# Optimization experiments

Measured on AMD Instinct MI355X. Metric: run time of the kernel, lower is better.

Reference implementation:

```python
import math
import jax, jax.numpy as jnp
import numpy as np

NUM_HEADS = 16
HIDDEN = 1024
HEAD_SIZE = HIDDEN // NUM_HEADS
B, S = 4, 2048


def setup_inputs() -> dict:
    key = jax.random.key(0)
    k1, k2, k3 = jax.random.split(key, 3)
    scale = 1.0 / math.sqrt(HIDDEN)
    return {
        "hidden_states": jax.random.normal(k1, (B, S, HIDDEN), dtype=jnp.float32),
        "attention_mask": jnp.ones((B, S), dtype=jnp.float32),
        "Wq": jax.random.normal(k2, (HIDDEN, HIDDEN), dtype=jnp.float32) * scale,
        "bq": jnp.zeros((HIDDEN,), dtype=jnp.float32),
        "Wk": jax.random.normal(k3, (HIDDEN, HIDDEN), dtype=jnp.float32) * scale,
        "bk": jnp.zeros((HIDDEN,), dtype=jnp.float32),
    }


def reference(hidden_states, attention_mask, Wq, bq, Wk, bk):
    b, s, _ = hidden_states.shape
    # Linear projections (torch Linear: x @ W.T + b)
    q = hidden_states @ Wq.T + bq  # [B,S,H]
    k = hidden_states @ Wk.T + bk  # [B,S,H]
    # split heads: [B, nH, S, dH]
    q = q.reshape(b, s, NUM_HEADS, HEAD_SIZE).transpose(0, 2, 1, 3)
    k = k.reshape(b, s, NUM_HEADS, HEAD_SIZE).transpose(0, 2, 1, 3)
    scores = jnp.einsum("bhqd,bhkd->bhqk", q, k)  # [B,nH,S,S]
    scores = scores / math.sqrt(HEAD_SIZE)  # sqrtatt=True
    scores = jnp.mean(scores, axis=1)  # aggregation='mean' -> [B,S,S]
    scores = scores * attention_mask[:, None, :]  # mask keys (cols)
    scores = scores * attention_mask[:, :, None]  # mask queries (rows)
    return scores
```

## Files before the change

### kernel.cpp

```cpp
#include <hip/hip_runtime.h>
#include <hip/hip_bf16.h>
#include <stdint.h>

#define S_LEN 2048
#define BATCH 4
#define HID 1024
#define M_ROWS (BATCH * S_LEN)

typedef __attribute__((ext_vector_type(8))) short short8;
typedef __attribute__((ext_vector_type(4))) float f32x4;

__device__ __forceinline__ void gload_lds16(const __hip_bfloat16* g,
                                            __hip_bfloat16* l) {
  __builtin_amdgcn_global_load_lds(
      (const __attribute__((address_space(1))) unsigned int*)g,
      (__attribute__((address_space(3))) unsigned int*)l, 16, 0, 0);
}

__global__ __launch_bounds__(256) void convert_all(
    const float* __restrict__ hs, const float* __restrict__ wq,
    const float* __restrict__ wk,
    __hip_bfloat16* __restrict__ hs_bf, __hip_bfloat16* __restrict__ wq_bf,
    __hip_bfloat16* __restrict__ wk_bf) {
  const int NH = M_ROWS * HID;
  const int NW = HID * HID;
  int idx = (blockIdx.x * blockDim.x + threadIdx.x) * 4;
  const float* src;
  __hip_bfloat16* dst;
  int off;
  if (idx < NH)           { src = hs; dst = hs_bf; off = idx; }
  else if (idx < NH + NW) { src = wq; dst = wq_bf; off = idx - NH; }
  else                    { src = wk; dst = wk_bf; off = idx - NH - NW; }
  float4 v = *reinterpret_cast<const float4*>(src + off);
  __hip_bfloat16 tmp[4];
  tmp[0] = __float2bfloat16(v.x);
  tmp[1] = __float2bfloat16(v.y);
  tmp[2] = __float2bfloat16(v.z);
  tmp[3] = __float2bfloat16(v.w);
  *reinterpret_cast<ushort4*>(dst + off) = *reinterpret_cast<const ushort4*>(tmp);
}

template <int NT>
__device__ __forceinline__ void gemm256_core(
    const __hip_bfloat16* __restrict__ A, const __hip_bfloat16* __restrict__ B,
    const int lda, const int ldb, __hip_bfloat16* lds, f32x4 acc[8][4]) {
  const int t = threadIdx.x;
  const int wid = t >> 6;
  const int l = t & 63;
  const int lr = l & 15;
  const int lk = l >> 4;
  const int wr = wid >> 2;
  const int wc = wid & 3;
  const int trow = t >> 3;
  const int tslot = (t & 7) ^ (trow & 7);
  const int rsx = lr & 7;

  __hip_bfloat16* const A0 = lds;
  __hip_bfloat16* const A1 = lds + 16384;
  __hip_bfloat16* const B0 = lds + 32768;
  __hip_bfloat16* const B1 = lds + 49152;

  short8 fa[4][2], fb[4][2];

#define STAGE_H(lb, gb, ld, half, kt) do {                                    \
    gload_lds16((gb) + (size_t)((half)*128 + 0  + trow) * (ld) + (kt)*64 +    \
                    tslot * 8,                                                \
                (lb) + ((half)*128 + 0) * 64 + wid * 512);                    \
    gload_lds16((gb) + (size_t)((half)*128 + 64 + trow) * (ld) + (kt)*64 +    \
                    tslot * 8,                                                \
                (lb) + ((half)*128 + 64) * 64 + wid * 512);                   \
  } while (0)

#define LDA_H(mh, Ac) do {                                                    \
    _Pragma("unroll") for (int m = 0; m < 4; ++m)                             \
    _Pragma("unroll") for (int kk = 0; kk < 2; ++kk)                          \
      fa[m][kk] = *reinterpret_cast<const short8*>(                           \
          (Ac) + (wr * 128 + (mh)*64 + m * 16 + lr) * 64 +                    \
          (((kk * 4 + lk) ^ rsx) * 8));                                       \
  } while (0)

#define LDB_H(nh, Bc) do {                                                    \
    _Pragma("unroll") for (int n = 0; n < 2; ++n)                             \
    _Pragma("unroll") for (int kk = 0; kk < 2; ++kk)                          \
      fb[(nh)*2 + n][kk] = *reinterpret_cast<const short8*>(                  \
          (Bc) + (wc * 64 + (nh)*32 + n * 16 + lr) * 64 +                     \
          (((kk * 4 + lk) ^ rsx) * 8));                                       \
  } while (0)

#define MFMA_Q(mh, nh) do {                                                   \
    __builtin_amdgcn_s_setprio(1);                                            \
    _Pragma("unroll") for (int m = 0; m < 4; ++m)                             \
    _Pragma("unroll") for (int n = 0; n < 2; ++n)                             \
    _Pragma("unroll") for (int kk = 0; kk < 2; ++kk)                          \
      acc[(mh)*4 + m][(nh)*2 + n] = __builtin_amdgcn_mfma_f32_16x16x32_bf16(  \
          fa[m][kk], fb[(nh)*2 + n][kk], acc[(mh)*4 + m][(nh)*2 + n], 0, 0, 0);\
    __builtin_amdgcn_s_setprio(0);                                            \
  } while (0)

#define CFENCE asm volatile("" ::: "memory")
#define BAR_PRE do { CFENCE; __builtin_amdgcn_s_barrier();                    \
    asm volatile("s_waitcnt lgkmcnt(0)" ::: "memory"); } while (0)
#define BAR_POST do { CFENCE; __builtin_amdgcn_s_barrier(); CFENCE; } while (0)

  STAGE_H(A0, A, lda, 0, 0); STAGE_H(A0, A, lda, 1, 0);
  STAGE_H(B0, B, ldb, 0, 0); STAGE_H(B0, B, ldb, 1, 0);
  STAGE_H(B1, B, ldb, 0, 1); STAGE_H(B1, B, ldb, 1, 1);
  asm volatile("s_waitcnt vmcnt(4)" ::: "memory");
  __builtin_amdgcn_s_barrier();
  CFENCE;

#pragma unroll 2
  for (int tt = 0; tt < NT; ++tt) {
    const int cur = tt & 1;
    __hip_bfloat16* const Ac = cur ? A1 : A0;
    __hip_bfloat16* const An = cur ? A0 : A1;
    __hip_bfloat16* const Bc = cur ? B1 : B0;
    LDA_H(0, Ac); LDB_H(0, Bc);
    if (tt + 1 < NT) STAGE_H(An, A, lda, 0, tt + 1);
    BAR_PRE; MFMA_Q(0, 0); BAR_POST;
    LDB_H(1, Bc);
    if (tt + 1 < NT) STAGE_H(An, A, lda, 1, tt + 1);
    BAR_PRE; MFMA_Q(0, 1); BAR_POST;
    LDA_H(1, Ac);
    if (tt + 2 < NT) STAGE_H(Bc, B, ldb, 0, tt + 2);
    BAR_PRE; MFMA_Q(1, 1); BAR_POST;
    if (tt + 2 < NT) STAGE_H(Bc, B, ldb, 1, tt + 2);
    BAR_PRE; MFMA_Q(1, 0);
    asm volatile("s_waitcnt vmcnt(4)" ::: "memory");
    BAR_POST;
  }
#undef STAGE_H
#undef LDA_H
#undef LDB_H
#undef MFMA_Q
#undef CFENCE
#undef BAR_PRE
#undef BAR_POST
}

__global__ __launch_bounds__(512, 2) void proj_gemm(
    const __hip_bfloat16* __restrict__ X,
    const __hip_bfloat16* __restrict__ Wq, const float* __restrict__ bq,
    const __hip_bfloat16* __restrict__ Wk, const float* __restrict__ bk,
    __hip_bfloat16* __restrict__ Qo, __hip_bfloat16* __restrict__ Ko) {
  extern __shared__ char smem[];
  __hip_bfloat16* lds = reinterpret_cast<__hip_bfloat16*>(smem);
  const __hip_bfloat16* W = (blockIdx.z == 0) ? Wq : Wk;
  const float* bias = (blockIdx.z == 0) ? bq : bk;
  __hip_bfloat16* Out = (blockIdx.z == 0) ? Qo : Ko;
  const int bm = blockIdx.y, bn = blockIdx.x;

  f32x4 acc[8][4];
#pragma unroll
  for (int m = 0; m < 8; ++m)
#pragma unroll
    for (int n = 0; n < 4; ++n) acc[m][n] = (f32x4){0.f, 0.f, 0.f, 0.f};

  gemm256_core<HID / 64>(X + (size_t)bm * 256 * HID,
                         W + (size_t)bn * 256 * HID, HID, HID, lds, acc);

  const int t = threadIdx.x, wid = t >> 6, l = t & 63;
  const int wr = wid >> 2, wc = wid & 3;
  const int lr = l & 15, lg = l >> 4;
#pragma unroll
  for (int m = 0; m < 8; ++m)
#pragma unroll
    for (int n = 0; n < 4; ++n) {
      const int col = bn * 256 + wc * 64 + n * 16 + lr;
      const float bb = bias[col];
#pragma unroll
      for (int r = 0; r < 4; ++r) {
        const int row = bm * 256 + wr * 128 + m * 16 + lg * 4 + r;
        Out[(size_t)row * HID + col] = __float2bfloat16(acc[m][n][r] + bb);
      }
    }
}

__global__ __launch_bounds__(512, 2) void scores_gemm(
    const __hip_bfloat16* __restrict__ Q, const __hip_bfloat16* __restrict__ Km,
    const float* __restrict__ mask, float* __restrict__ out) {
  extern __shared__ char smem[];
  __hip_bfloat16* lds = reinterpret_cast<__hip_bfloat16*>(smem);
  const int b = blockIdx.z;
  const int bm = blockIdx.y, bn = blockIdx.x;

  f32x4 acc[8][4];
#pragma unroll
  for (int m = 0; m < 8; ++m)
#pragma unroll
    for (int n = 0; n < 4; ++n) acc[m][n] = (f32x4){0.f, 0.f, 0.f, 0.f};

  gemm256_core<HID / 64>(Q + ((size_t)b * S_LEN + bm * 256) * HID,
                         Km + ((size_t)b * S_LEN + bn * 256) * HID, HID, HID,
                         lds, acc);

  const int t = threadIdx.x, wid = t >> 6, l = t & 63;
  const int wr = wid >> 2, wc = wid & 3;
  const int lr = l & 15, lg = l >> 4;
  const float inv = 1.0f / 128.0f;
#pragma unroll
  for (int m = 0; m < 8; ++m)
#pragma unroll
    for (int n = 0; n < 4; ++n) {
      const int col = bn * 256 + wc * 64 + n * 16 + lr;
      const float mc = mask[b * S_LEN + col] * inv;
#pragma unroll
      for (int r = 0; r < 4; ++r) {
        const int row = bm * 256 + wr * 128 + m * 16 + lg * 4 + r;
        const float mr = mask[b * S_LEN + row];
        out[(size_t)b * S_LEN * S_LEN + (size_t)row * S_LEN + col] =
            acc[m][n][r] * mc * mr;
      }
    }
}

extern "C" void kernel_launch(void* const* d_in, const int* in_sizes, int n_in,
                              void* d_out, int out_size, void* d_ws,
                              size_t ws_size, hipStream_t stream) {
  const float* hs   = (const float*)d_in[0];
  const float* mask = (const float*)d_in[1];
  const float* Wq   = (const float*)d_in[2];
  const float* bq   = (const float*)d_in[3];
  const float* Wk   = (const float*)d_in[4];
  const float* bk   = (const float*)d_in[5];
  float* out = (float*)d_out;

  char* ws = (char*)d_ws;
  __hip_bfloat16* hs_bf = (__hip_bfloat16*)(ws);
  __hip_bfloat16* wq_bf = (__hip_bfloat16*)(ws + 16777216);
  __hip_bfloat16* wk_bf = (__hip_bfloat16*)(ws + 18874368);
  __hip_bfloat16* q_bf  = (__hip_bfloat16*)(ws + 20971520);
  __hip_bfloat16* k_bf  = (__hip_bfloat16*)(ws + 37748736);

  (void)hipFuncSetAttribute((const void*)proj_gemm,
                            hipFuncAttributeMaxDynamicSharedMemorySize, 131072);
  (void)hipFuncSetAttribute((const void*)scores_gemm,
                            hipFuncAttributeMaxDynamicSharedMemorySize, 131072);

  hipLaunchKernelGGL(convert_all, dim3(10240), dim3(256), 0, stream,
                     hs, Wq, Wk, hs_bf, wq_bf, wk_bf);
  hipLaunchKernelGGL(proj_gemm, dim3(HID / 256, M_ROWS / 256, 2), dim3(512),
                     131072, stream, hs_bf, wq_bf, bq, wk_bf, bk, q_bf, k_bf);
  hipLaunchKernelGGL(scores_gemm, dim3(S_LEN / 256, S_LEN / 256, BATCH),
                     dim3(512), 131072, stream, q_bf, k_bf, mask, out);
}
```

Measured before the change: 90.01 us.

## Fold Wq^T·Wk into one mid matrix to replace separate Q/K projections

Averaging over heads makes the score matrix equal to the full 1024-wide dot product of Q and K. That product is rewritten as X·(Wq^T Wk)·X^T plus rank-one bias terms. A small 1024x1024 product builds the mid matrix, split over K into four partials that are then reduced. One projection GEMM produces T, and the scores GEMM multiplies T by the bf16 hidden states, adding row and column bias vectors in the epilogue. This removes one of the two large projection GEMMs, at the cost of several extra small kernels and bf16 rounding of the combined weight matrix.

Result: slower. 105.2 us (+16.9%).

```diff
diff --git a/kernel.cpp b/kernel.cpp
--- a/kernel.cpp
+++ b/kernel.cpp
@@ -17,33 +17,101 @@
       (__attribute__((address_space(3))) unsigned int*)l, 16, 0, 0);
 }
 
-__global__ __launch_bounds__(256) void convert_all(
-    const float* __restrict__ hs, const float* __restrict__ wq,
-    const float* __restrict__ wk,
-    __hip_bfloat16* __restrict__ hs_bf, __hip_bfloat16* __restrict__ wq_bf,
-    __hip_bfloat16* __restrict__ wk_bf) {
-  const int NH = M_ROWS * HID;
-  const int NW = HID * HID;
-  int idx = (blockIdx.x * blockDim.x + threadIdx.x) * 4;
-  const float* src;
-  __hip_bfloat16* dst;
-  int off;
-  if (idx < NH)           { src = hs; dst = hs_bf; off = idx; }
-  else if (idx < NH + NW) { src = wq; dst = wq_bf; off = idx - NH; }
-  else                    { src = wk; dst = wk_bf; off = idx - NH - NW; }
-  float4 v = *reinterpret_cast<const float4*>(src + off);
-  __hip_bfloat16 tmp[4];
-  tmp[0] = __float2bfloat16(v.x);
-  tmp[1] = __float2bfloat16(v.y);
-  tmp[2] = __float2bfloat16(v.z);
-  tmp[3] = __float2bfloat16(v.w);
-  *reinterpret_cast<ushort4*>(dst + off) = *reinterpret_cast<const ushort4*>(tmp);
-}
-
-template <int NT>
-__device__ __forceinline__ void gemm256_core(
+template <int N>
+__device__ __forceinline__ void wait_vm() {
+  if constexpr (N == 0)
+    asm volatile("s_waitcnt vmcnt(0)" ::: "memory");
+  else if constexpr (N == 2)
+    asm volatile("s_waitcnt vmcnt(2)" ::: "memory");
+  else
+    asm volatile("s_waitcnt vmcnt(4)" ::: "memory");
+}
+
+__global__ __launch_bounds__(256) void transpose_convert(
+    const float* __restrict__ Wq, const float* __restrict__ Wk,
+    __hip_bfloat16* __restrict__ WqT, __hip_bfloat16* __restrict__ WkT) {
+  __shared__ float tile[32][33];
+  const float* src = blockIdx.z ? Wk : Wq;
+  __hip_bfloat16* dst = blockIdx.z ? WkT : WqT;
+  const int tx = threadIdx.x & 31, ty = threadIdx.x >> 5;
+  const int r0 = blockIdx.y * 32, c0 = blockIdx.x * 32;
+#pragma unroll
+  for (int rr = 0; rr < 4; ++rr) {
+    const int r = ty + rr * 8;
+    tile[r][tx] = src[(size_t)(r0 + r) * HID + c0 + tx];
+  }
+  __syncthreads();
+#pragma unroll
+  for (int rr = 0; rr < 4; ++rr) {
+    const int r = ty + rr * 8;
+    dst[(size_t)(c0 + r) * HID + r0 + tx] = __float2bfloat16(tile[tx][r]);
+  }
+}
+
+__global__ __launch_bounds__(256) void bias_stage1(
+    const __hip_bfloat16* __restrict__ WqT,
+    const __hip_bfloat16* __restrict__ WkT, const float* __restrict__ bq,
+    const float* __restrict__ bk, float* __restrict__ a1,
+    float* __restrict__ a2, float* __restrict__ cbuf) {
+  const int g = blockIdx.x * 4 + (threadIdx.x >> 6);
+  const int l = threadIdx.x & 63;
+  const int mat = g & 1;
+  const int j = g >> 1;
+  const __hip_bfloat16* W = mat ? WkT : WqT;
+  const float* bv = mat ? bq : bk;
+  float s = 0.f;
+#pragma unroll
+  for (int e = 0; e < 16; ++e)
+    s += __bfloat162float(W[(size_t)j * HID + l * 16 + e]) * bv[l * 16 + e];
+#pragma unroll
+  for (int m = 1; m < 64; m <<= 1) s += __shfl_xor(s, m, 64);
+  if (l == 0) (mat ? a2 : a1)[j] = s;
+  if (blockIdx.x == 0 && threadIdx.x < 64) {
+    float cs = 0.f;
+#pragma unroll
+    for (int e = 0; e < 16; ++e)
+      cs += bq[threadIdx.x * 16 + e] * bk[threadIdx.x * 16 + e];
+#pragma unroll
+    for (int m = 1; m < 64; m <<= 1) cs += __shfl_xor(cs, m, 64);
+    if (threadIdx.x == 0) cbuf[0] = cs;
+  }
+}
+
+__global__ __launch_bounds__(256) void convert_hs(
+    const float* __restrict__ hs, const float* __restrict__ a1,
+    const float* __restrict__ a2, const float* __restrict__ cbuf,
+    __hip_bfloat16* __restrict__ hs_bf, float* __restrict__ u,
+    float* __restrict__ w) {
+  const int i = blockIdx.x;
+  const int t = threadIdx.x;
+  float4 v = *reinterpret_cast<const float4*>(hs + (size_t)i * HID + t * 4);
+  __hip_bfloat16 tmp[4] = {__float2bfloat16(v.x), __float2bfloat16(v.y),
+                           __float2bfloat16(v.z), __float2bfloat16(v.w)};
+  *reinterpret_cast<ushort4*>(hs_bf + (size_t)i * HID + t * 4) =
+      *reinterpret_cast<const ushort4*>(tmp);
+  float4 A1 = *reinterpret_cast<const float4*>(a1 + t * 4);
+  float4 A2 = *reinterpret_cast<const float4*>(a2 + t * 4);
+  float pu = v.x * A1.x + v.y * A1.y + v.z * A1.z + v.w * A1.w;
+  float pw = v.x * A2.x + v.y * A2.y + v.z * A2.z + v.w * A2.w;
+#pragma unroll
+  for (int m = 1; m < 64; m <<= 1) {
+    pu += __shfl_xor(pu, m, 64);
+    pw += __shfl_xor(pw, m, 64);
+  }
+  __shared__ float su[4], sw[4];
+  if ((t & 63) == 0) { su[t >> 6] = pu; sw[t >> 6] = pw; }
+  __syncthreads();
+  if (t == 0) {
+    u[i] = su[0] + su[1] + su[2] + su[3] + cbuf[0];
+    w[i] = sw[0] + sw[1] + sw[2] + sw[3];
+  }
+}
+
+template <int NT, int NF>
+__device__ __forceinline__ void gemm_core(
     const __hip_bfloat16* __restrict__ A, const __hip_bfloat16* __restrict__ B,
-    const int lda, const int ldb, __hip_bfloat16* lds, f32x4 acc[8][4]) {
+    const int lda, const int ldb, __hip_bfloat16* lds, f32x4 acc[8][NF]) {
+  constexpr int NH = NF / 2;
   const int t = threadIdx.x;
   const int wid = t >> 6;
   const int l = t & 63;
@@ -58,11 +126,11 @@
   __hip_bfloat16* const A0 = lds;
   __hip_bfloat16* const A1 = lds + 16384;
   __hip_bfloat16* const B0 = lds + 32768;
-  __hip_bfloat16* const B1 = lds + 49152;
-
-  short8 fa[4][2], fb[4][2];
-
-#define STAGE_H(lb, gb, ld, half, kt) do {                                    \
+  __hip_bfloat16* const B1 = B0 + NF * 64 * 64;
+
+  short8 fa[4][2], fb[NF][2];
+
+#define STAGE_U(lb, gb, ld, half, kt) do {                                    \
     gload_lds16((gb) + (size_t)((half)*128 + 0  + trow) * (ld) + (kt)*64 +    \
                     tslot * 8,                                                \
                 (lb) + ((half)*128 + 0) * 64 + wid * 512);                    \
@@ -80,20 +148,21 @@
   } while (0)
 
 #define LDB_H(nh, Bc) do {                                                    \
-    _Pragma("unroll") for (int n = 0; n < 2; ++n)                             \
+    _Pragma("unroll") for (int n = 0; n < NH; ++n)                            \
     _Pragma("unroll") for (int kk = 0; kk < 2; ++kk)                          \
-      fb[(nh)*2 + n][kk] = *reinterpret_cast<const short8*>(                  \
-          (Bc) + (wc * 64 + (nh)*32 + n * 16 + lr) * 64 +                     \
+      fb[(nh)*NH + n][kk] = *reinterpret_cast<const short8*>(                 \
+          (Bc) + (wc * (NF * 16) + (nh) * (NH * 16) + n * 16 + lr) * 64 +     \
           (((kk * 4 + lk) ^ rsx) * 8));                                       \
   } while (0)
 
 #define MFMA_Q(mh, nh) do {                                                   \
     __builtin_amdgcn_s_setprio(1);                                            \
     _Pragma("unroll") for (int m = 0; m < 4; ++m)                             \
-    _Pragma("unroll") for (int n = 0; n < 2; ++n)                             \
+    _Pragma("unroll") for (int n = 0; n < NH; ++n)                            \
     _Pragma("unroll") for (int kk = 0; kk < 2; ++kk)                          \
-      acc[(mh)*4 + m][(nh)*2 + n] = __builtin_amdgcn_mfma_f32_16x16x32_bf16(  \
-          fa[m][kk], fb[(nh)*2 + n][kk], acc[(mh)*4 + m][(nh)*2 + n], 0, 0, 0);\
+      acc[(mh)*4 + m][(nh)*NH + n] = __builtin_amdgcn_mfma_f32_16x16x32_bf16( \
+          fa[m][kk], fb[(nh)*NH + n][kk], acc[(mh)*4 + m][(nh)*NH + n],       \
+          0, 0, 0);                                                           \
     __builtin_amdgcn_s_setprio(0);                                            \
   } while (0)
 
@@ -102,10 +171,10 @@
     asm volatile("s_waitcnt lgkmcnt(0)" ::: "memory"); } while (0)
 #define BAR_POST do { CFENCE; __builtin_amdgcn_s_barrier(); CFENCE; } while (0)
 
-  STAGE_H(A0, A, lda, 0, 0); STAGE_H(A0, A, lda, 1, 0);
-  STAGE_H(B0, B, ldb, 0, 0); STAGE_H(B0, B, ldb, 1, 0);
-  STAGE_H(B1, B, ldb, 0, 1); STAGE_H(B1, B, ldb, 1, 1);
-  asm volatile("s_waitcnt vmcnt(4)" ::: "memory");
+  STAGE_U(A0, A, lda, 0, 0); STAGE_U(A0, A, lda, 1, 0);
+  STAGE_U(B0, B, ldb, 0, 0); if (NH == 2) STAGE_U(B0, B, ldb, 1, 0);
+  STAGE_U(B1, B, ldb, 0, 1); if (NH == 2) STAGE_U(B1, B, ldb, 1, 1);
+  wait_vm<2 * NH>();
   __builtin_amdgcn_s_barrier();
   CFENCE;
 
@@ -116,20 +185,20 @@
     __hip_bfloat16* const An = cur ? A0 : A1;
     __hip_bfloat16* const Bc = cur ? B1 : B0;
     LDA_H(0, Ac); LDB_H(0, Bc);
-    if (tt + 1 < NT) STAGE_H(An, A, lda, 0, tt + 1);
+    if (tt + 1 < NT) STAGE_U(An, A, lda, 0, tt + 1);
     BAR_PRE; MFMA_Q(0, 0); BAR_POST;
     LDB_H(1, Bc);
-    if (tt + 1 < NT) STAGE_H(An, A, lda, 1, tt + 1);
+    if (tt + 1 < NT) STAGE_U(An, A, lda, 1, tt + 1);
     BAR_PRE; MFMA_Q(0, 1); BAR_POST;
     LDA_H(1, Ac);
-    if (tt + 2 < NT) STAGE_H(Bc, B, ldb, 0, tt + 2);
+    if (tt + 2 < NT) STAGE_U(Bc, B, ldb, 0, tt + 2);
     BAR_PRE; MFMA_Q(1, 1); BAR_POST;
-    if (tt + 2 < NT) STAGE_H(Bc, B, ldb, 1, tt + 2);
+    if (NH == 2 && tt + 2 < NT) STAGE_U(Bc, B, ldb, 1, tt + 2);
     BAR_PRE; MFMA_Q(1, 0);
-    asm volatile("s_waitcnt vmcnt(4)" ::: "memory");
+    if (tt + 2 < NT) wait_vm<2 * NH>(); else wait_vm<0>();
     BAR_POST;
   }
-#undef STAGE_H
+#undef STAGE_U
 #undef LDA_H
 #undef LDB_H
 #undef MFMA_Q
@@ -138,47 +207,90 @@
 #undef BAR_POST
 }
 
-__global__ __launch_bounds__(512, 2) void proj_gemm(
-    const __hip_bfloat16* __restrict__ X,
-    const __hip_bfloat16* __restrict__ Wq, const float* __restrict__ bq,
-    const __hip_bfloat16* __restrict__ Wk, const float* __restrict__ bk,
-    __hip_bfloat16* __restrict__ Qo, __hip_bfloat16* __restrict__ Ko) {
+__global__ __launch_bounds__(512, 2) void wmid_gemm(
+    const __hip_bfloat16* __restrict__ WkT,
+    const __hip_bfloat16* __restrict__ WqT, float* __restrict__ part) {
   extern __shared__ char smem[];
   __hip_bfloat16* lds = reinterpret_cast<__hip_bfloat16*>(smem);
-  const __hip_bfloat16* W = (blockIdx.z == 0) ? Wq : Wk;
-  const float* bias = (blockIdx.z == 0) ? bq : bk;
-  __hip_bfloat16* Out = (blockIdx.z == 0) ? Qo : Ko;
-  const int bm = blockIdx.y, bn = blockIdx.x;
-
+  const int kz = blockIdx.z;
   f32x4 acc[8][4];
 #pragma unroll
   for (int m = 0; m < 8; ++m)
 #pragma unroll
     for (int n = 0; n < 4; ++n) acc[m][n] = (f32x4){0.f, 0.f, 0.f, 0.f};
 
-  gemm256_core<HID / 64>(X + (size_t)bm * 256 * HID,
-                         W + (size_t)bn * 256 * HID, HID, HID, lds, acc);
-
+  gemm_core<4, 4>(WkT + (size_t)blockIdx.y * 256 * HID + kz * 256,
+                  WqT + (size_t)blockIdx.x * 256 * HID + kz * 256, HID, HID,
+                  lds, acc);
+
+  float* outp = part + (size_t)kz * (HID * HID);
   const int t = threadIdx.x, wid = t >> 6, l = t & 63;
-  const int wr = wid >> 2, wc = wid & 3;
+  const int wr = wid >> 2, wcn = wid & 3;
   const int lr = l & 15, lg = l >> 4;
 #pragma unroll
   for (int m = 0; m < 8; ++m)
 #pragma unroll
     for (int n = 0; n < 4; ++n) {
-      const int col = bn * 256 + wc * 64 + n * 16 + lr;
-      const float bb = bias[col];
+      const int col = blockIdx.x * 256 + wcn * 64 + n * 16 + lr;
 #pragma unroll
       for (int r = 0; r < 4; ++r) {
-        const int row = bm * 256 + wr * 128 + m * 16 + lg * 4 + r;
-        Out[(size_t)row * HID + col] = __float2bfloat16(acc[m][n][r] + bb);
+        const int row = blockIdx.y * 256 + wr * 128 + m * 16 + lg * 4 + r;
+        outp[(size_t)row * HID + col] = acc[m][n][r];
       }
     }
 }
 
+__global__ __launch_bounds__(256) void wmid_reduce(
+    const float* __restrict__ part, __hip_bfloat16* __restrict__ wmid_bf) {
+  const int idx = (blockIdx.x * 256 + threadIdx.x) * 4;
+  float4 s0 = *reinterpret_cast<const float4*>(part + idx);
+  float4 s1 = *reinterpret_cast<const float4*>(part + (HID * HID) + idx);
+  float4 s2 = *reinterpret_cast<const float4*>(part + 2 * (HID * HID) + idx);
+  float4 s3 = *reinterpret_cast<const float4*>(part + 3 * (HID * HID) + idx);
+  __hip_bfloat16 tmp[4] = {__float2bfloat16(s0.x + s1.x + s2.x + s3.x),
+                           __float2bfloat16(s0.y + s1.y + s2.y + s3.y),
+                           __float2bfloat16(s0.z + s1.z + s2.z + s3.z),
+                           __float2bfloat16(s0.w + s1.w + s2.w + s3.w)};
+  *reinterpret_cast<ushort4*>(wmid_bf + idx) =
+      *reinterpret_cast<const ushort4*>(tmp);
+}
+
+__global__ __launch_bounds__(512, 2) void t_gemm(
+    const __hip_bfloat16* __restrict__ hs_bf,
+    const __hip_bfloat16* __restrict__ wmid_bf,
+    __hip_bfloat16* __restrict__ T) {
+  extern __shared__ char smem[];
+  __hip_bfloat16* lds = reinterpret_cast<__hip_bfloat16*>(smem);
+  f32x4 acc[8][2];
+#pragma unroll
+  for (int m = 0; m < 8; ++m)
+#pragma unroll
+    for (int n = 0; n < 2; ++n) acc[m][n] = (f32x4){0.f, 0.f, 0.f, 0.f};
+
+  gemm_core<16, 2>(hs_bf + (size_t)blockIdx.y * 256 * HID,
+                   wmid_bf + (size_t)blockIdx.x * 128 * HID, HID, HID, lds,
+                   acc);
+
+  const int t = threadIdx.x, wid = t >> 6, l = t & 63;
+  const int wr = wid >> 2, wcn = wid & 3;
+  const int lr = l & 15, lg = l >> 4;
+#pragma unroll
+  for (int m = 0; m < 8; ++m)
+#pragma unroll
+    for (int n = 0; n < 2; ++n) {
+      const int col = blockIdx.x * 128 + wcn * 32 + n * 16 + lr;
+#pragma unroll
+      for (int r = 0; r < 4; ++r) {
+        const int row = blockIdx.y * 256 + wr * 128 + m * 16 + lg * 4 + r;
+        T[(size_t)row * HID + col] = __float2bfloat16(acc[m][n][r]);
+      }
+    }
+}
+
 __global__ __launch_bounds__(512, 2) void scores_gemm(
-    const __hip_bfloat16* __restrict__ Q, const __hip_bfloat16* __restrict__ Km,
-    const float* __restrict__ mask, float* __restrict__ out) {
+    const __hip_bfloat16* __restrict__ T, const __hip_bfloat16* __restrict__ hs_bf,
+    const float* __restrict__ mask, const float* __restrict__ u,
+    const float* __restrict__ w, float* __restrict__ out) {
   extern __shared__ char smem[];
   __hip_bfloat16* lds = reinterpret_cast<__hip_bfloat16*>(smem);
   const int b = blockIdx.z;
@@ -190,26 +302,28 @@
 #pragma unroll
     for (int n = 0; n < 4; ++n) acc[m][n] = (f32x4){0.f, 0.f, 0.f, 0.f};
 
-  gemm256_core<HID / 64>(Q + ((size_t)b * S_LEN + bm * 256) * HID,
-                         Km + ((size_t)b * S_LEN + bn * 256) * HID, HID, HID,
-                         lds, acc);
+  gemm_core<16, 4>(T + ((size_t)b * S_LEN + bm * 256) * HID,
+                   hs_bf + ((size_t)b * S_LEN + bn * 256) * HID, HID, HID,
+                   lds, acc);
 
   const int t = threadIdx.x, wid = t >> 6, l = t & 63;
-  const int wr = wid >> 2, wc = wid & 3;
+  const int wr = wid >> 2, wcn = wid & 3;
   const int lr = l & 15, lg = l >> 4;
   const float inv = 1.0f / 128.0f;
 #pragma unroll
   for (int m = 0; m < 8; ++m)
 #pragma unroll
     for (int n = 0; n < 4; ++n) {
-      const int col = bn * 256 + wc * 64 + n * 16 + lr;
-      const float mc = mask[b * S_LEN + col] * inv;
+      const int col = bn * 256 + wcn * 64 + n * 16 + lr;
+      const float mc = mask[b * S_LEN + col];
+      const float wadd = w[b * S_LEN + col];
 #pragma unroll
       for (int r = 0; r < 4; ++r) {
         const int row = bm * 256 + wr * 128 + m * 16 + lg * 4 + r;
         const float mr = mask[b * S_LEN + row];
+        const float uadd = u[b * S_LEN + row];
         out[(size_t)b * S_LEN * S_LEN + (size_t)row * S_LEN + col] =
-            acc[m][n][r] * mc * mr;
+            (acc[m][n][r] + uadd + wadd) * inv * mc * mr;
       }
     }
 }
@@ -226,21 +340,38 @@
   float* out = (float*)d_out;
 
   char* ws = (char*)d_ws;
-  __hip_bfloat16* hs_bf = (__hip_bfloat16*)(ws);
-  __hip_bfloat16* wq_bf = (__hip_bfloat16*)(ws + 16777216);
-  __hip_bfloat16* wk_bf = (__hip_bfloat16*)(ws + 18874368);
-  __hip_bfloat16* q_bf  = (__hip_bfloat16*)(ws + 20971520);
-  __hip_bfloat16* k_bf  = (__hip_bfloat16*)(ws + 37748736);
-
-  (void)hipFuncSetAttribute((const void*)proj_gemm,
+  __hip_bfloat16* hs_bf   = (__hip_bfloat16*)(ws);
+  float*          wmid_p  = (float*)(ws + 16777216);
+  __hip_bfloat16* T_bf    = (__hip_bfloat16*)(ws + 16777216);
+  __hip_bfloat16* WqT     = (__hip_bfloat16*)(ws + 33554432);
+  __hip_bfloat16* WkT     = (__hip_bfloat16*)(ws + 35651584);
+  __hip_bfloat16* wmid_bf = (__hip_bfloat16*)(ws + 37748736);
+  float*          a1      = (float*)(ws + 39845888);
+  float*          a2      = (float*)(ws + 39849984);
+  float*          cbuf    = (float*)(ws + 39854080);
+  float*          uvec    = (float*)(ws + 39858176);
+  float*          wvec    = (float*)(ws + 39890944);
+
+  (void)hipFuncSetAttribute((const void*)wmid_gemm,
                             hipFuncAttributeMaxDynamicSharedMemorySize, 131072);
+  (void)hipFuncSetAttribute((const void*)t_gemm,
+                            hipFuncAttributeMaxDynamicSharedMemorySize, 98304);
   (void)hipFuncSetAttribute((const void*)scores_gemm,
                             hipFuncAttributeMaxDynamicSharedMemorySize, 131072);
 
-  hipLaunchKernelGGL(convert_all, dim3(10240), dim3(256), 0, stream,
-                     hs, Wq, Wk, hs_bf, wq_bf, wk_bf);
-  hipLaunchKernelGGL(proj_gemm, dim3(HID / 256, M_ROWS / 256, 2), dim3(512),
-                     131072, stream, hs_bf, wq_bf, bq, wk_bf, bk, q_bf, k_bf);
+  hipLaunchKernelGGL(transpose_convert, dim3(32, 32, 2), dim3(256), 0, stream,
+                     Wq, Wk, WqT, WkT);
+  hipLaunchKernelGGL(bias_stage1, dim3(512), dim3(256), 0, stream,
+                     WqT, WkT, bq, bk, a1, a2, cbuf);
+  hipLaunchKernelGGL(convert_hs, dim3(M_ROWS), dim3(256), 0, stream,
+                     hs, a1, a2, cbuf, hs_bf, uvec, wvec);
+  hipLaunchKernelGGL(wmid_gemm, dim3(4, 4, 4), dim3(512), 131072, stream,
+                     WkT, WqT, wmid_p);
+  hipLaunchKernelGGL(wmid_reduce, dim3(1024), dim3(256), 0, stream,
+                     wmid_p, wmid_bf);
+  hipLaunchKernelGGL(t_gemm, dim3(HID / 128, M_ROWS / 256), dim3(512), 98304,
+                     stream, hs_bf, wmid_bf, T_bf);
   hipLaunchKernelGGL(scores_gemm, dim3(S_LEN / 256, S_LEN / 256, BATCH),
-                     dim3(512), 131072, stream, q_bf, k_bf, mask, out);
-}
+                     dim3(512), 131072, stream, T_bf, hs_bf, mask, uvec, wvec,
+                     out);
+}
```

## Switch GEMMs to 32x32x16 MFMA and remap blocks for XCD-local reuse

Applied to the files above, without the earlier changes.

Both GEMMs now use the 32x32x16 bf16 MFMA instead of 16x16x32. This halves the number of MFMA issues and LDS fragment reads per tile, and the register fragments and epilogue indexing are changed to match the 32x32 output layout. Launch grids become 1D, with a block-id remap that groups tiles sharing A/B panels onto the same XCD to improve L2 reuse. The final loop iteration now drains vmcnt to 0. Epilogue store patterns change and register pressure rises with the larger accumulators.

Measured after the change: 98.65 us. 1.1x slower.

```diff
diff --git a/kernel.cpp b/kernel.cpp
--- a/kernel.cpp
+++ b/kernel.cpp
@@ -8,13 +8,21 @@
 #define M_ROWS (BATCH * S_LEN)
 
 typedef __attribute__((ext_vector_type(8))) short short8;
-typedef __attribute__((ext_vector_type(4))) float f32x4;
+typedef __attribute__((ext_vector_type(16))) float f32x16;
 
 __device__ __forceinline__ void gload_lds16(const __hip_bfloat16* g,
                                             __hip_bfloat16* l) {
   __builtin_amdgcn_global_load_lds(
       (const __attribute__((address_space(1))) unsigned int*)g,
       (__attribute__((address_space(3))) unsigned int*)l, 16, 0, 0);
+}
+
+template <int N>
+__device__ __forceinline__ void wait_vm() {
+  if constexpr (N == 0)
+    asm volatile("s_waitcnt vmcnt(0)" ::: "memory");
+  else
+    asm volatile("s_waitcnt vmcnt(4)" ::: "memory");
 }
 
 __global__ __launch_bounds__(256) void convert_all(
@@ -41,28 +49,28 @@
 }
 
 template <int NT>
-__device__ __forceinline__ void gemm256_core(
+__device__ __forceinline__ void gemm_core32(
     const __hip_bfloat16* __restrict__ A, const __hip_bfloat16* __restrict__ B,
-    const int lda, const int ldb, __hip_bfloat16* lds, f32x4 acc[8][4]) {
+    const int lda, const int ldb, __hip_bfloat16* lds, f32x16 acc[4][2]) {
   const int t = threadIdx.x;
   const int wid = t >> 6;
   const int l = t & 63;
-  const int lr = l & 15;
-  const int lk = l >> 4;
+  const int lr32 = l & 31;
+  const int hk = l >> 5;
   const int wr = wid >> 2;
   const int wc = wid & 3;
   const int trow = t >> 3;
   const int tslot = (t & 7) ^ (trow & 7);
-  const int rsx = lr & 7;
+  const int rsx = lr32 & 7;
 
   __hip_bfloat16* const A0 = lds;
   __hip_bfloat16* const A1 = lds + 16384;
   __hip_bfloat16* const B0 = lds + 32768;
   __hip_bfloat16* const B1 = lds + 49152;
 
-  short8 fa[4][2], fb[4][2];
-
-#define STAGE_H(lb, gb, ld, half, kt) do {                                    \
+  short8 fa[2][4], fb[2][4];
+
+#define STAGE_U(lb, gb, ld, half, kt) do {                                    \
     gload_lds16((gb) + (size_t)((half)*128 + 0  + trow) * (ld) + (kt)*64 +    \
                     tslot * 8,                                                \
                 (lb) + ((half)*128 + 0) * 64 + wid * 512);                    \
@@ -71,29 +79,27 @@
                 (lb) + ((half)*128 + 64) * 64 + wid * 512);                   \
   } while (0)
 
-#define LDA_H(mh, Ac) do {                                                    \
-    _Pragma("unroll") for (int m = 0; m < 4; ++m)                             \
-    _Pragma("unroll") for (int kk = 0; kk < 2; ++kk)                          \
-      fa[m][kk] = *reinterpret_cast<const short8*>(                           \
-          (Ac) + (wr * 128 + (mh)*64 + m * 16 + lr) * 64 +                    \
-          (((kk * 4 + lk) ^ rsx) * 8));                                       \
-  } while (0)
-
-#define LDB_H(nh, Bc) do {                                                    \
-    _Pragma("unroll") for (int n = 0; n < 2; ++n)                             \
-    _Pragma("unroll") for (int kk = 0; kk < 2; ++kk)                          \
-      fb[(nh)*2 + n][kk] = *reinterpret_cast<const short8*>(                  \
-          (Bc) + (wc * 64 + (nh)*32 + n * 16 + lr) * 64 +                     \
-          (((kk * 4 + lk) ^ rsx) * 8));                                       \
+#define LDA2(mh, Ac) do {                                                     \
+    _Pragma("unroll") for (int mm = 0; mm < 2; ++mm)                          \
+    _Pragma("unroll") for (int kk = 0; kk < 4; ++kk)                          \
+      fa[mm][kk] = *reinterpret_cast<const short8*>(                          \
+          (Ac) + (wr * 128 + ((mh)*2 + mm) * 32 + lr32) * 64 +                \
+          (((kk * 2 + hk) ^ rsx) * 8));                                       \
+  } while (0)
+
+#define LDB1(nh, Bc) do {                                                     \
+    _Pragma("unroll") for (int kk = 0; kk < 4; ++kk)                          \
+      fb[nh][kk] = *reinterpret_cast<const short8*>(                          \
+          (Bc) + (wc * 64 + (nh)*32 + lr32) * 64 +                            \
+          (((kk * 2 + hk) ^ rsx) * 8));                                       \
   } while (0)
 
 #define MFMA_Q(mh, nh) do {                                                   \
     __builtin_amdgcn_s_setprio(1);                                            \
-    _Pragma("unroll") for (int m = 0; m < 4; ++m)                             \
-    _Pragma("unroll") for (int n = 0; n < 2; ++n)                             \
-    _Pragma("unroll") for (int kk = 0; kk < 2; ++kk)                          \
-      acc[(mh)*4 + m][(nh)*2 + n] = __builtin_amdgcn_mfma_f32_16x16x32_bf16(  \
-          fa[m][kk], fb[(nh)*2 + n][kk], acc[(mh)*4 + m][(nh)*2 + n], 0, 0, 0);\
+    _Pragma("unroll") for (int mm = 0; mm < 2; ++mm)                          \
+    _Pragma("unroll") for (int kk = 0; kk < 4; ++kk)                          \
+      acc[(mh)*2 + mm][nh] = __builtin_amdgcn_mfma_f32_32x32x16_bf16(         \
+          fa[mm][kk], fb[nh][kk], acc[(mh)*2 + mm][nh], 0, 0, 0);             \
     __builtin_amdgcn_s_setprio(0);                                            \
   } while (0)
 
@@ -102,10 +108,10 @@
     asm volatile("s_waitcnt lgkmcnt(0)" ::: "memory"); } while (0)
 #define BAR_POST do { CFENCE; __builtin_amdgcn_s_barrier(); CFENCE; } while (0)
 
-  STAGE_H(A0, A, lda, 0, 0); STAGE_H(A0, A, lda, 1, 0);
-  STAGE_H(B0, B, ldb, 0, 0); STAGE_H(B0, B, ldb, 1, 0);
-  STAGE_H(B1, B, ldb, 0, 1); STAGE_H(B1, B, ldb, 1, 1);
-  asm volatile("s_waitcnt vmcnt(4)" ::: "memory");
+  STAGE_U(A0, A, lda, 0, 0); STAGE_U(A0, A, lda, 1, 0);
+  STAGE_U(B0, B, ldb, 0, 0); STAGE_U(B0, B, ldb, 1, 0);
+  STAGE_U(B1, B, ldb, 0, 1); STAGE_U(B1, B, ldb, 1, 1);
+  wait_vm<4>();
   __builtin_amdgcn_s_barrier();
   CFENCE;
 
@@ -115,23 +121,23 @@
     __hip_bfloat16* const Ac = cur ? A1 : A0;
     __hip_bfloat16* const An = cur ? A0 : A1;
     __hip_bfloat16* const Bc = cur ? B1 : B0;
-    LDA_H(0, Ac); LDB_H(0, Bc);
-    if (tt + 1 < NT) STAGE_H(An, A, lda, 0, tt + 1);
+    LDA2(0, Ac); LDB1(0, Bc);
+    if (tt + 1 < NT) STAGE_U(An, A, lda, 0, tt + 1);
     BAR_PRE; MFMA_Q(0, 0); BAR_POST;
-    LDB_H(1, Bc);
-    if (tt + 1 < NT) STAGE_H(An, A, lda, 1, tt + 1);
+    LDB1(1, Bc);
+    if (tt + 1 < NT) STAGE_U(An, A, lda, 1, tt + 1);
     BAR_PRE; MFMA_Q(0, 1); BAR_POST;
-    LDA_H(1, Ac);
-    if (tt + 2 < NT) STAGE_H(Bc, B, ldb, 0, tt + 2);
+    LDA2(1, Ac);
+    if (tt + 2 < NT) STAGE_U(Bc, B, ldb, 0, tt + 2);
     BAR_PRE; MFMA_Q(1, 1); BAR_POST;
-    if (tt + 2 < NT) STAGE_H(Bc, B, ldb, 1, tt + 2);
+    if (tt + 2 < NT) STAGE_U(Bc, B, ldb, 1, tt + 2);
     BAR_PRE; MFMA_Q(1, 0);
-    asm volatile("s_waitcnt vmcnt(4)" ::: "memory");
+    if (tt + 2 < NT) wait_vm<4>(); else wait_vm<0>();
     BAR_POST;
   }
-#undef STAGE_H
-#undef LDA_H
-#undef LDB_H
+#undef STAGE_U
+#undef LDA2
+#undef LDB1
 #undef MFMA_Q
 #undef CFENCE
 #undef BAR_PRE
@@ -145,35 +151,45 @@
     __hip_bfloat16* __restrict__ Qo, __hip_bfloat16* __restrict__ Ko) {
   extern __shared__ char smem[];
   __hip_bfloat16* lds = reinterpret_cast<__hip_bfloat16*>(smem);
-  const __hip_bfloat16* W = (blockIdx.z == 0) ? Wq : Wk;
-  const float* bias = (blockIdx.z == 0) ? bq : bk;
-  __hip_bfloat16* Out = (blockIdx.z == 0) ? Qo : Ko;
-  const int bm = blockIdx.y, bn = blockIdx.x;
-
-  f32x4 acc[8][4];
-#pragma unroll
-  for (int m = 0; m < 8; ++m)
-#pragma unroll
-    for (int n = 0; n < 4; ++n) acc[m][n] = (f32x4){0.f, 0.f, 0.f, 0.f};
-
-  gemm256_core<HID / 64>(X + (size_t)bm * 256 * HID,
-                         W + (size_t)bn * 256 * HID, HID, HID, lds, acc);
+  const int bid = blockIdx.x;
+  const int xcd = bid & 7, s = bid >> 3;
+  const int bm = xcd * 4 + (s & 3);
+  const int bn8 = s >> 2;
+  const int z = bn8 >> 2;
+  const int bn = bn8 & 3;
+
+  const __hip_bfloat16* W = z ? Wk : Wq;
+  const float* bias = z ? bk : bq;
+  __hip_bfloat16* Out = z ? Ko : Qo;
+
+  f32x16 acc[4][2];
+#pragma unroll
+  for (int mi = 0; mi < 4; ++mi)
+#pragma unroll
+    for (int ni = 0; ni < 2; ++ni)
+#pragma unroll
+      for (int e = 0; e < 16; ++e) acc[mi][ni][e] = 0.f;
+
+  gemm_core32<HID / 64>(X + (size_t)bm * 256 * HID,
+                        W + (size_t)bn * 256 * HID, HID, HID, lds, acc);
 
   const int t = threadIdx.x, wid = t >> 6, l = t & 63;
   const int wr = wid >> 2, wc = wid & 3;
-  const int lr = l & 15, lg = l >> 4;
-#pragma unroll
-  for (int m = 0; m < 8; ++m)
-#pragma unroll
-    for (int n = 0; n < 4; ++n) {
-      const int col = bn * 256 + wc * 64 + n * 16 + lr;
-      const float bb = bias[col];
-#pragma unroll
-      for (int r = 0; r < 4; ++r) {
-        const int row = bm * 256 + wr * 128 + m * 16 + lg * 4 + r;
-        Out[(size_t)row * HID + col] = __float2bfloat16(acc[m][n][r] + bb);
+  const int lr32 = l & 31, hk = l >> 5;
+#pragma unroll
+  for (int ni = 0; ni < 2; ++ni) {
+    const int col = bn * 256 + wc * 64 + ni * 32 + lr32;
+    const float bb = bias[col];
+#pragma unroll
+    for (int mi = 0; mi < 4; ++mi) {
+#pragma unroll
+      for (int reg = 0; reg < 16; ++reg) {
+        const int row =
+            bm * 256 + wr * 128 + mi * 32 + (reg & 3) + 8 * (reg >> 2) + 4 * hk;
+        Out[(size_t)row * HID + col] = __float2bfloat16(acc[mi][ni][reg] + bb);
       }
     }
+  }
 }
 
 __global__ __launch_bounds__(512, 2) void scores_gemm(
@@ -181,37 +197,44 @@
     const float* __restrict__ mask, float* __restrict__ out) {
   extern __shared__ char smem[];
   __hip_bfloat16* lds = reinterpret_cast<__hip_bfloat16*>(smem);
-  const int b = blockIdx.z;
-  const int bm = blockIdx.y, bn = blockIdx.x;
-
-  f32x4 acc[8][4];
-#pragma unroll
-  for (int m = 0; m < 8; ++m)
-#pragma unroll
-    for (int n = 0; n < 4; ++n) acc[m][n] = (f32x4){0.f, 0.f, 0.f, 0.f};
-
-  gemm256_core<HID / 64>(Q + ((size_t)b * S_LEN + bm * 256) * HID,
-                         Km + ((size_t)b * S_LEN + bn * 256) * HID, HID, HID,
-                         lds, acc);
+  const int bid = blockIdx.x;
+  const int xcd = bid & 7, slot = bid >> 3;
+  const int b = slot >> 3, sub = slot & 7;
+  const int bm = (xcd & 3) * 2 + (sub >> 2);
+  const int bn = (xcd >> 2) * 4 + (sub & 3);
+
+  f32x16 acc[4][2];
+#pragma unroll
+  for (int mi = 0; mi < 4; ++mi)
+#pragma unroll
+    for (int ni = 0; ni < 2; ++ni)
+#pragma unroll
+      for (int e = 0; e < 16; ++e) acc[mi][ni][e] = 0.f;
+
+  gemm_core32<HID / 64>(Q + ((size_t)b * S_LEN + bm * 256) * HID,
+                        Km + ((size_t)b * S_LEN + bn * 256) * HID, HID, HID,
+                        lds, acc);
 
   const int t = threadIdx.x, wid = t >> 6, l = t & 63;
   const int wr = wid >> 2, wc = wid & 3;
-  const int lr = l & 15, lg = l >> 4;
+  const int lr32 = l & 31, hk = l >> 5;
   const float inv = 1.0f / 128.0f;
 #pragma unroll
-  for (int m = 0; m < 8; ++m)
-#pragma unroll
-    for (int n = 0; n < 4; ++n) {
-      const int col = bn * 256 + wc * 64 + n * 16 + lr;
-      const float mc = mask[b * S_LEN + col] * inv;
-#pragma unroll
-      for (int r = 0; r < 4; ++r) {
-        const int row = bm * 256 + wr * 128 + m * 16 + lg * 4 + r;
+  for (int ni = 0; ni < 2; ++ni) {
+    const int col = bn * 256 + wc * 64 + ni * 32 + lr32;
+    const float mc = mask[b * S_LEN + col];
+#pragma unroll
+    for (int mi = 0; mi < 4; ++mi) {
+#pragma unroll
+      for (int reg = 0; reg < 16; ++reg) {
+        const int row =
+            bm * 256 + wr * 128 + mi * 32 + (reg & 3) + 8 * (reg >> 2) + 4 * hk;
         const float mr = mask[b * S_LEN + row];
         out[(size_t)b * S_LEN * S_LEN + (size_t)row * S_LEN + col] =
-            acc[m][n][r] * mc * mr;
+            acc[mi][ni][reg] * inv * mr * mc;
       }
     }
+  }
 }
 
 extern "C" void kernel_launch(void* const* d_in, const int* in_sizes, int n_in,
@@ -239,8 +262,8 @@
 
   hipLaunchKernelGGL(convert_all, dim3(10240), dim3(256), 0, stream,
                      hs, Wq, Wk, hs_bf, wq_bf, wk_bf);
-  hipLaunchKernelGGL(proj_gemm, dim3(HID / 256, M_ROWS / 256, 2), dim3(512),
-                     131072, stream, hs_bf, wq_bf, bq, wk_bf, bk, q_bf, k_bf);
-  hipLaunchKernelGGL(scores_gemm, dim3(S_LEN / 256, S_LEN / 256, BATCH),
-                     dim3(512), 131072, stream, q_bf, k_bf, mask, out);
-}
+  hipLaunchKernelGGL(proj_gemm, dim3(256), dim3(512), 131072, stream,
+                     hs_bf, wq_bf, bq, wk_bf, bk, q_bf, k_bf);
+  hipLaunchKernelGGL(scores_gemm, dim3(256), dim3(512), 131072, stream,
+                     q_bf, k_bf, mask, out);
+}
```

## Transpose MFMA operands for vectorized epilogue stores and XCD-aware block swizzle

Applied to the files above, without the earlier changes.

Swaps the A/B operands of the MFMA so each lane holds four consecutive columns, which lets both GEMM epilogues write with 16-byte vector stores (nontemporal for the fp32 score output) instead of scattered scalar stores. Both GEMM grids are flattened to 1D and remapped so blocks sharing operand tiles land on the same XCD, aiming at better L2 reuse. The final iteration now drains all outstanding loads with vmcnt(0). The remapping assumes round-robin block dispatch across 8 XCDs.

New measurement: 96.50 us. +7.2%, slower.

```diff
diff --git a/kernel.cpp b/kernel.cpp
--- a/kernel.cpp
+++ b/kernel.cpp
@@ -10,12 +10,24 @@
 typedef __attribute__((ext_vector_type(8))) short short8;
 typedef __attribute__((ext_vector_type(4))) float f32x4;
 
-__device__ __forceinline__ void gload_lds16(const __hip_bfloat16* g,
-                                            __hip_bfloat16* l) {
+__device__ __forceinline__ void gload_lds16(const void* g, void* l) {
   __builtin_amdgcn_global_load_lds(
       (const __attribute__((address_space(1))) unsigned int*)g,
       (__attribute__((address_space(3))) unsigned int*)l, 16, 0, 0);
 }
+
+template <int N>
+__device__ __forceinline__ void wait_vm() {
+  if constexpr (N == 0)
+    asm volatile("s_waitcnt vmcnt(0)" ::: "memory");
+  else
+    asm volatile("s_waitcnt vmcnt(4)" ::: "memory");
+}
+
+#define CFENCE asm volatile("" ::: "memory")
+#define BAR_PRE do { CFENCE; __builtin_amdgcn_s_barrier();                    \
+    asm volatile("s_waitcnt lgkmcnt(0)" ::: "memory"); } while (0)
+#define BAR_POST do { CFENCE; __builtin_amdgcn_s_barrier(); CFENCE; } while (0)
 
 __global__ __launch_bounds__(256) void convert_all(
     const float* __restrict__ hs, const float* __restrict__ wq,
@@ -41,7 +53,7 @@
 }
 
 template <int NT>
-__device__ __forceinline__ void gemm256_core(
+__device__ __forceinline__ void gemm_core_bf(
     const __hip_bfloat16* __restrict__ A, const __hip_bfloat16* __restrict__ B,
     const int lda, const int ldb, __hip_bfloat16* lds, f32x4 acc[8][4]) {
   const int t = threadIdx.x;
@@ -62,7 +74,7 @@
 
   short8 fa[4][2], fb[4][2];
 
-#define STAGE_H(lb, gb, ld, half, kt) do {                                    \
+#define STAGE_U(lb, gb, ld, half, kt) do {                                    \
     gload_lds16((gb) + (size_t)((half)*128 + 0  + trow) * (ld) + (kt)*64 +    \
                     tslot * 8,                                                \
                 (lb) + ((half)*128 + 0) * 64 + wid * 512);                    \
@@ -93,19 +105,15 @@
     _Pragma("unroll") for (int n = 0; n < 2; ++n)                             \
     _Pragma("unroll") for (int kk = 0; kk < 2; ++kk)                          \
       acc[(mh)*4 + m][(nh)*2 + n] = __builtin_amdgcn_mfma_f32_16x16x32_bf16(  \
-          fa[m][kk], fb[(nh)*2 + n][kk], acc[(mh)*4 + m][(nh)*2 + n], 0, 0, 0);\
+          fb[(nh)*2 + n][kk], fa[m][kk], acc[(mh)*4 + m][(nh)*2 + n],         \
+          0, 0, 0);                                                           \
     __builtin_amdgcn_s_setprio(0);                                            \
   } while (0)
 
-#define CFENCE asm volatile("" ::: "memory")
-#define BAR_PRE do { CFENCE; __builtin_amdgcn_s_barrier();                    \
-    asm volatile("s_waitcnt lgkmcnt(0)" ::: "memory"); } while (0)
-#define BAR_POST do { CFENCE; __builtin_amdgcn_s_barrier(); CFENCE; } while (0)
-
-  STAGE_H(A0, A, lda, 0, 0); STAGE_H(A0, A, lda, 1, 0);
-  STAGE_H(B0, B, ldb, 0, 0); STAGE_H(B0, B, ldb, 1, 0);
-  STAGE_H(B1, B, ldb, 0, 1); STAGE_H(B1, B, ldb, 1, 1);
-  asm volatile("s_waitcnt vmcnt(4)" ::: "memory");
+  STAGE_U(A0, A, lda, 0, 0); STAGE_U(A0, A, lda, 1, 0);
+  STAGE_U(B0, B, ldb, 0, 0); STAGE_U(B0, B, ldb, 1, 0);
+  STAGE_U(B1, B, ldb, 0, 1); STAGE_U(B1, B, ldb, 1, 1);
+  wait_vm<4>();
   __builtin_amdgcn_s_barrier();
   CFENCE;
 
@@ -116,26 +124,23 @@
     __hip_bfloat16* const An = cur ? A0 : A1;
     __hip_bfloat16* const Bc = cur ? B1 : B0;
     LDA_H(0, Ac); LDB_H(0, Bc);
-    if (tt + 1 < NT) STAGE_H(An, A, lda, 0, tt + 1);
+    if (tt + 1 < NT) STAGE_U(An, A, lda, 0, tt + 1);
     BAR_PRE; MFMA_Q(0, 0); BAR_POST;
     LDB_H(1, Bc);
-    if (tt + 1 < NT) STAGE_H(An, A, lda, 1, tt + 1);
+    if (tt + 1 < NT) STAGE_U(An, A, lda, 1, tt + 1);
     BAR_PRE; MFMA_Q(0, 1); BAR_POST;
     LDA_H(1, Ac);
-    if (tt + 2 < NT) STAGE_H(Bc, B, ldb, 0, tt + 2);
+    if (tt + 2 < NT) STAGE_U(Bc, B, ldb, 0, tt + 2);
     BAR_PRE; MFMA_Q(1, 1); BAR_POST;
-    if (tt + 2 < NT) STAGE_H(Bc, B, ldb, 1, tt + 2);
+    if (tt + 2 < NT) STAGE_U(Bc, B, ldb, 1, tt + 2);
     BAR_PRE; MFMA_Q(1, 0);
-    asm volatile("s_waitcnt vmcnt(4)" ::: "memory");
+    if (tt + 2 < NT) wait_vm<4>(); else wait_vm<0>();
     BAR_POST;
   }
-#undef STAGE_H
+#undef STAGE_U
 #undef LDA_H
 #undef LDB_H
 #undef MFMA_Q
-#undef CFENCE
-#undef BAR_PRE
-#undef BAR_POST
 }
 
 __global__ __launch_bounds__(512, 2) void proj_gemm(
@@ -145,10 +150,16 @@
     __hip_bfloat16* __restrict__ Qo, __hip_bfloat16* __restrict__ Ko) {
   extern __shared__ char smem[];
   __hip_bfloat16* lds = reinterpret_cast<__hip_bfloat16*>(smem);
-  const __hip_bfloat16* W = (blockIdx.z == 0) ? Wq : Wk;
-  const float* bias = (blockIdx.z == 0) ? bq : bk;
-  __hip_bfloat16* Out = (blockIdx.z == 0) ? Qo : Ko;
-  const int bm = blockIdx.y, bn = blockIdx.x;
+  const int bid = blockIdx.x;
+  const int xcd = bid & 7, s = bid >> 3;
+  const int bm = xcd * 4 + (s & 3);
+  const int bn8 = s >> 2;
+  const int z = bn8 >> 2;
+  const int bn = bn8 & 3;
+
+  const __hip_bfloat16* W = z ? Wk : Wq;
+  const float* bias = z ? bk : bq;
+  __hip_bfloat16* Out = z ? Ko : Qo;
 
   f32x4 acc[8][4];
 #pragma unroll
@@ -156,24 +167,27 @@
 #pragma unroll
     for (int n = 0; n < 4; ++n) acc[m][n] = (f32x4){0.f, 0.f, 0.f, 0.f};
 
-  gemm256_core<HID / 64>(X + (size_t)bm * 256 * HID,
+  gemm_core_bf<HID / 64>(X + (size_t)bm * 256 * HID,
                          W + (size_t)bn * 256 * HID, HID, HID, lds, acc);
 
   const int t = threadIdx.x, wid = t >> 6, l = t & 63;
   const int wr = wid >> 2, wc = wid & 3;
   const int lr = l & 15, lg = l >> 4;
 #pragma unroll
-  for (int m = 0; m < 8; ++m)
+  for (int m = 0; m < 8; ++m) {
+    const int row = bm * 256 + wr * 128 + m * 16 + lr;
 #pragma unroll
     for (int n = 0; n < 4; ++n) {
-      const int col = bn * 256 + wc * 64 + n * 16 + lr;
-      const float bb = bias[col];
-#pragma unroll
-      for (int r = 0; r < 4; ++r) {
-        const int row = bm * 256 + wr * 128 + m * 16 + lg * 4 + r;
-        Out[(size_t)row * HID + col] = __float2bfloat16(acc[m][n][r] + bb);
-      }
+      const int col0 = bn * 256 + wc * 64 + n * 16 + lg * 4;
+      float4 bb = *reinterpret_cast<const float4*>(&bias[col0]);
+      f32x4 a = acc[m][n];
+      __hip_bfloat16 tmp[4] = {
+          __float2bfloat16(a[0] + bb.x), __float2bfloat16(a[1] + bb.y),
+          __float2bfloat16(a[2] + bb.z), __float2bfloat16(a[3] + bb.w)};
+      *reinterpret_cast<ushort4*>(&Out[(size_t)row * HID + col0]) =
+          *reinterpret_cast<const ushort4*>(tmp);
     }
+  }
 }
 
 __global__ __launch_bounds__(512, 2) void scores_gemm(
@@ -181,8 +195,11 @@
     const float* __restrict__ mask, float* __restrict__ out) {
   extern __shared__ char smem[];
   __hip_bfloat16* lds = reinterpret_cast<__hip_bfloat16*>(smem);
-  const int b = blockIdx.z;
-  const int bm = blockIdx.y, bn = blockIdx.x;
+  const int bid = blockIdx.x;
+  const int xcd = bid & 7, slot = bid >> 3;
+  const int b = slot >> 3, sub = slot & 7;
+  const int bm = (xcd & 3) * 2 + (sub >> 2);
+  const int bn = (xcd >> 2) * 4 + (sub & 3);
 
   f32x4 acc[8][4];
 #pragma unroll
@@ -190,7 +207,7 @@
 #pragma unroll
     for (int n = 0; n < 4; ++n) acc[m][n] = (f32x4){0.f, 0.f, 0.f, 0.f};
 
-  gemm256_core<HID / 64>(Q + ((size_t)b * S_LEN + bm * 256) * HID,
+  gemm_core_bf<HID / 64>(Q + ((size_t)b * S_LEN + bm * 256) * HID,
                          Km + ((size_t)b * S_LEN + bn * 256) * HID, HID, HID,
                          lds, acc);
 
@@ -199,19 +216,21 @@
   const int lr = l & 15, lg = l >> 4;
   const float inv = 1.0f / 128.0f;
 #pragma unroll
-  for (int m = 0; m < 8; ++m)
+  for (int m = 0; m < 8; ++m) {
+    const int row = bm * 256 + wr * 128 + m * 16 + lr;
+    const float mr = mask[b * S_LEN + row] * inv;
 #pragma unroll
     for (int n = 0; n < 4; ++n) {
-      const int col = bn * 256 + wc * 64 + n * 16 + lr;
-      const float mc = mask[b * S_LEN + col] * inv;
-#pragma unroll
-      for (int r = 0; r < 4; ++r) {
-        const int row = bm * 256 + wr * 128 + m * 16 + lg * 4 + r;
-        const float mr = mask[b * S_LEN + row];
-        out[(size_t)b * S_LEN * S_LEN + (size_t)row * S_LEN + col] =
-            acc[m][n][r] * mc * mr;
-      }
+      const int col0 = bn * 256 + wc * 64 + n * 16 + lg * 4;
+      float4 mcv = *reinterpret_cast<const float4*>(&mask[b * S_LEN + col0]);
+      f32x4 a = acc[m][n];
+      f32x4 o = {a[0] * mr * mcv.x, a[1] * mr * mcv.y,
+                 a[2] * mr * mcv.z, a[3] * mr * mcv.w};
+      __builtin_nontemporal_store(
+          o, reinterpret_cast<f32x4*>(
+                 &out[(size_t)b * S_LEN * S_LEN + (size_t)row * S_LEN + col0]));
     }
+  }
 }
 
 extern "C" void kernel_launch(void* const* d_in, const int* in_sizes, int n_in,
@@ -239,8 +258,8 @@
 
   hipLaunchKernelGGL(convert_all, dim3(10240), dim3(256), 0, stream,
                      hs, Wq, Wk, hs_bf, wq_bf, wk_bf);
-  hipLaunchKernelGGL(proj_gemm, dim3(HID / 256, M_ROWS / 256, 2), dim3(512),
-                     131072, stream, hs_bf, wq_bf, bq, wk_bf, bk, q_bf, k_bf);
-  hipLaunchKernelGGL(scores_gemm, dim3(S_LEN / 256, S_LEN / 256, BATCH),
-                     dim3(512), 131072, stream, q_bf, k_bf, mask, out);
-}
+  hipLaunchKernelGGL(proj_gemm, dim3(256), dim3(512), 131072, stream,
+                     hs_bf, wq_bf, bq, wk_bf, bk, q_bf, k_bf);
+  hipLaunchKernelGGL(scores_gemm, dim3(256), dim3(512), 131072, stream,
+                     q_bf, k_bf, mask, out);
+}
```
